# Kernel tuning notes

Hardware: AMD Instinct MI355X
Metric: run time of the kernel (lower is better)

The kernel has to match this reference:

```python
import jax, jax.numpy as jnp
import numpy as np

WEIGHT = 1.0
BOND_CUTOFF = 2.4


def setup_inputs() -> dict:
    key = jax.random.key(0)
    k0, k1, k2, k3, k4, k5 = jax.random.split(key, 6)
    N_TOK, L, B = 512, 3072, 2
    is_ligand = jax.random.randint(k0, (N_TOK,), 0, 2) > 0
    token_bonds = jax.random.randint(k1, (N_TOK, N_TOK), 0, 2) > 0
    atom_to_token_map = jax.random.randint(k2, (L,), 0, N_TOK, dtype=jnp.int32)
    crd_mask_L = jax.random.randint(k3, (B, L), 0, 2) > 0
    X_L = jax.random.normal(k4, (B, L, 3), dtype=jnp.float32)
    X_gt_L = jax.random.normal(k5, (B, L, 3), dtype=jnp.float32)
    return {
        'is_ligand': is_ligand,
        'token_bonds': token_bonds,
        'atom_to_token_map': atom_to_token_map,
        'crd_mask_L': crd_mask_L,
        'X_L': X_L,
        'X_gt_L': X_gt_L,
    }


def _pairwise_sqdist(X):
    # X: [B, L, 3] -> [B, L, L] squared pairwise distances
    d = X[:, :, None, :] - X[:, None, :, :]
    return jnp.sum(d * d, axis=-1)


def reference(is_ligand, token_bonds, atom_to_token_map, crd_mask_L, X_L, X_gt_L):
    # inter-polymer-ligand token pair mask: ligand i, non-ligand j
    inter = is_ligand[:, None] & (~is_ligand)[None, :]          # [T, T]
    pl_bonds = token_bonds & inter                              # [T, T]
    # The original O(n_bonds * L^2) loop is exactly this gather:
    pl_atoms = pl_bonds[atom_to_token_map[:, None], atom_to_token_map[None, :]]  # [L, L]
    crd_mask_LL = crd_mask_L[:, :, None] & crd_mask_L[:, None, :]                # [B, L, L]
    mask = pl_atoms[None, :, :] & crd_mask_LL                                    # [B, L, L]

    # safe sqrt (masked entries set to 1 before sqrt; excluded from loss anyway)
    pred = jnp.sqrt(jnp.where(mask, _pairwise_sqdist(X_L), 1.0))
    gt = jnp.sqrt(jnp.where(mask, _pairwise_sqdist(X_gt_L), 1.0))

    bonded = mask & (gt < BOND_CUTOFF)
    err2 = jnp.where(bonded, jnp.square(pred - gt), 0.0)
    cnt = jnp.maximum(jnp.sum(bonded), 1)
    loss = jnp.sum(err2) / cnt.astype(err2.dtype)
    return (WEIGHT * loss, loss)
```

## Files before the change

### kernel.cpp

```cpp
#include <hip/hip_runtime.h>

#define L 3072
#define NT 512
#define CUT2 5.76f
#define GRID 256
#define BLOCK 1024
#define MAXRPB 12

typedef unsigned int u32;
typedef unsigned long long u64;

__global__ __launch_bounds__(BLOCK) void plbl_main(
    const int* __restrict__ is_ligand,
    const int* __restrict__ token_bonds,
    const int* __restrict__ tokmap,
    const int* __restrict__ crd,
    const float* __restrict__ X,
    const float* __restrict__ Xgt,
    double* __restrict__ part_sum,
    u32* __restrict__ part_cnt)
{
    const int t = threadIdx.x;
    const int lane = t & 63;
    const int wv = t >> 6;

    __shared__ u64 s_lig[8];
    __shared__ u32 s_wtot[2][16];
    __shared__ u32 s_cnts[2];
    __shared__ u32 s_colmeta[3072];
    __shared__ u32 s_rowlist[3072];
    __shared__ u64 s_bond[MAXRPB][8];
    __shared__ __align__(16) float s_rowc[MAXRPB][12];
    __shared__ u32 s_rbits[MAXRPB];
    __shared__ double s_rsum[16];
    __shared__ u32 s_rcnt[16];

    if (t < NT) {
        const bool v = is_ligand[t] != 0;
        const u64 bal = __ballot(v);
        if (lane == 0) s_lig[wv] = bal;
    }
    __syncthreads();

    u32 cc = 0, rc = 0;
    u32 meta[3];
    bool cok[3], rok[3];
    #pragma unroll
    for (int k = 0; k < 3; k++) {
        const int a = t * 3 + k;
        const u32 tok = (u32)tokmap[a];
        const bool lig = (s_lig[tok >> 6] >> (tok & 63)) & 1ULL;
        const u32 m0 = crd[a] != 0;
        const u32 m1 = crd[L + a] != 0;
        const bool any = (m0 | m1) != 0u;
        meta[k] = (u32)a | (tok << 12) | (m0 << 21) | (m1 << 22);
        cok[k] = (!lig) && any;
        rok[k] = lig && any;
        cc += cok[k] ? 1u : 0u;
        rc += rok[k] ? 1u : 0u;
    }

    u32 ci = cc, ri = rc;
    #pragma unroll
    for (int o = 1; o < 64; o <<= 1) {
        u32 cv = __shfl_up(ci, o, 64);
        u32 rv = __shfl_up(ri, o, 64);
        if (lane >= o) { ci += cv; ri += rv; }
    }
    if (lane == 63) { s_wtot[0][wv] = ci; s_wtot[1][wv] = ri; }
    __syncthreads();

    if (wv == 0 && lane < 16) {
        const u32 c = s_wtot[0][lane];
        const u32 r = s_wtot[1][lane];
        u32 cs = c, rs = r;
        #pragma unroll
        for (int o = 1; o < 16; o <<= 1) {
            u32 cv = __shfl_up(cs, o, 64);
            u32 rv = __shfl_up(rs, o, 64);
            if (lane >= o) { cs += cv; rs += rv; }
        }
        s_wtot[0][lane] = cs - c;
        s_wtot[1][lane] = rs - r;
        if (lane == 15) { s_cnts[0] = cs; s_cnts[1] = rs; }
    }
    __syncthreads();

    u32 coff = s_wtot[0][wv] + (ci - cc);
    u32 roff = s_wtot[1][wv] + (ri - rc);
    #pragma unroll
    for (int k = 0; k < 3; k++) {
        if (cok[k]) s_colmeta[coff++] = meta[k];
        if (rok[k]) s_rowlist[roff++] = meta[k];
    }
    __syncthreads();

    const int ncol = (int)s_cnts[0];
    const int nrow = (int)s_cnts[1];

    const int rpb = (nrow + GRID - 1) / GRID;
    const int r0 = blockIdx.x * rpb;
    const int r1 = (r0 + rpb < nrow) ? (r0 + rpb) : nrow;
    const int nr = (r1 > r0) ? (r1 - r0) : 0;

    for (int r = 0; r < nr; r++) {
        const u32 rm = s_rowlist[r0 + r];
        const u32 ta1 = (rm >> 12) & 0x1FF;
        if (t < NT) {
            const bool bv = token_bonds[ta1 * NT + t] != 0;
            const u64 bal = __ballot(bv);
            if (lane == 0) s_bond[r][wv] = bal;
        }
    }
    if (t < nr * 12) {
        const int r = t / 12, c = t % 12;
        const u32 rm = s_rowlist[r0 + r];
        const int a1 = (int)(rm & 0xFFF);
        const int batch = (c % 6) / 3;
        const int axis  = c % 3;
        const float* src = (c < 6) ? X : Xgt;
        s_rowc[r][c] = src[(batch * L + a1) * 3 + axis];
    }
    if (t < nr) s_rbits[t] = (s_rowlist[r0 + t] >> 21) & 3u;
    __syncthreads();

    double acc = 0.0;
    u32 cnt = 0;

    for (int j = t; j < ncol; j += BLOCK) {
        const u32 cm = s_colmeta[j];
        const int a2 = (int)(cm & 0xFFF);
        const u32 tok = (cm >> 12) & 0x1FF;
        const u32 cbits = (cm >> 21) & 3u;
        const u32 bhi = tok >> 6;
        const u64 bsel = 1ULL << (tok & 63);

        const int b0 = 3 * a2;
        const int b1 = 3 * L + 3 * a2;
        const float vx0 = X[b0 + 0], vy0 = X[b0 + 1], vz0 = X[b0 + 2];
        const float vx1 = X[b1 + 0], vy1 = X[b1 + 1], vz1 = X[b1 + 2];
        const float wx0 = Xgt[b0 + 0], wy0 = Xgt[b0 + 1], wz0 = Xgt[b0 + 2];
        const float wx1 = Xgt[b1 + 0], wy1 = Xgt[b1 + 1], wz1 = Xgt[b1 + 2];

        for (int r = 0; r < nr; r++) {
            const bool bond = (s_bond[r][bhi] & bsel) != 0ULL;
            const u32 mb = s_rbits[r] & cbits;

            const float p0x = s_rowc[r][0], p0y = s_rowc[r][1], p0z = s_rowc[r][2];
            const float p1x = s_rowc[r][3], p1y = s_rowc[r][4], p1z = s_rowc[r][5];
            const float g0x = s_rowc[r][6], g0y = s_rowc[r][7], g0z = s_rowc[r][8];
            const float g1x = s_rowc[r][9], g1y = s_rowc[r][10], g1z = s_rowc[r][11];

            const float dgx0 = g0x - wx0, dgy0 = g0y - wy0, dgz0 = g0z - wz0;
            const float gt2_0 = dgx0 * dgx0 + dgy0 * dgy0 + dgz0 * dgz0;
            const float dpx0 = p0x - vx0, dpy0 = p0y - vy0, dpz0 = p0z - vz0;
            const float pr2_0 = dpx0 * dpx0 + dpy0 * dpy0 + dpz0 * dpz0;
            const float d0 = sqrtf(pr2_0) - sqrtf(gt2_0);
            const bool k0 = bond && (mb & 1u) && (gt2_0 < CUT2);
            const float dgx1 = g1x - wx1, dgy1 = g1y - wy1, dgz1 = g1z - wz1;
            const float gt2_1 = dgx1 * dgx1 + dgy1 * dgy1 + dgz1 * dgz1;
            const float dpx1 = p1x - vx1, dpy1 = p1y - vy1, dpz1 = p1z - vz1;
            const float pr2_1 = dpx1 * dpx1 + dpy1 * dpy1 + dpz1 * dpz1;
            const float d1 = sqrtf(pr2_1) - sqrtf(gt2_1);
            const bool k1 = bond && (mb & 2u) && (gt2_1 < CUT2);

            const float e = (k0 ? d0 * d0 : 0.0f) + (k1 ? d1 * d1 : 0.0f);
            acc += (double)e;
            cnt += (k0 ? 1u : 0u) + (k1 ? 1u : 0u);
        }
    }

    #pragma unroll
    for (int o = 32; o > 0; o >>= 1) {
        acc += __shfl_down(acc, o, 64);
        cnt += __shfl_down(cnt, o, 64);
    }
    if (lane == 0) { s_rsum[wv] = acc; s_rcnt[wv] = cnt; }
    __syncthreads();
    if (t == 0) {
        double a = 0.0;
        u32 c = 0;
        #pragma unroll
        for (int i = 0; i < 16; i++) { a += s_rsum[i]; c += s_rcnt[i]; }
        part_sum[blockIdx.x] = a;
        part_cnt[blockIdx.x] = c;
    }
}

__global__ __launch_bounds__(256) void plbl_fin(
    const double* __restrict__ part_sum,
    const u32* __restrict__ part_cnt,
    float* __restrict__ out)
{
    const int t = threadIdx.x;
    const int lane = t & 63;
    const int wv = t >> 6;
    double a = part_sum[t];
    u32 c = part_cnt[t];
    #pragma unroll
    for (int o = 32; o > 0; o >>= 1) {
        a += __shfl_down(a, o, 64);
        c += __shfl_down(c, o, 64);
    }
    __shared__ double s_sum[4];
    __shared__ u32 s_cnt[4];
    if (lane == 0) { s_sum[wv] = a; s_cnt[wv] = c; }
    __syncthreads();
    if (t == 0) {
        const double sum = s_sum[0] + s_sum[1] + s_sum[2] + s_sum[3];
        const u32 cc = s_cnt[0] + s_cnt[1] + s_cnt[2] + s_cnt[3];
        const u32 n = cc ? cc : 1u;
        const float loss = (float)(sum / (double)n);
        out[0] = loss;
        out[1] = loss;
    }
}

extern "C" void kernel_launch(void* const* d_in, const int* in_sizes, int n_in,
                              void* d_out, int out_size, void* d_ws, size_t ws_size,
                              hipStream_t stream) {
    const int*   is_ligand   = (const int*)d_in[0];
    const int*   token_bonds = (const int*)d_in[1];
    const int*   tokmap      = (const int*)d_in[2];
    const int*   crd_mask    = (const int*)d_in[3];
    const float* X           = (const float*)d_in[4];
    const float* Xgt         = (const float*)d_in[5];
    float* out = (float*)d_out;

    char* w = (char*)d_ws;
    double* part_sum = (double*)(w + 0);
    u32*    part_cnt = (u32*)(w + 8 * GRID);

    plbl_main<<<GRID, BLOCK, 0, stream>>>(is_ligand, token_bonds, tokmap,
                                          crd_mask, X, Xgt,
                                          part_sum, part_cnt);
    plbl_fin<<<1, 256, 0, stream>>>(part_sum, part_cnt, out);
}
```

Before: 16.66 us.

## Fuse final reduction into main kernel via cooperative grid sync

Merges the separate finalize kernel into the main kernel, using a cooperative launch and grid-wide sync so that block 0 reduces the per-block partials and writes the loss. It also replaces one block barrier in the prefix scan with per-wave shuffles, and splits the token-bond ballot loading across both halves of the block. The aim is to remove a second kernel launch and some block synchronisation. In exchange it adds cooperative-launch overhead and a grid barrier across 256 blocks of 1024 threads.

After: 52.67 us. +216.1%, slower.

```diff
diff --git a/kernel.cpp b/kernel.cpp
--- a/kernel.cpp
+++ b/kernel.cpp
@@ -1,4 +1,7 @@
 #include <hip/hip_runtime.h>
+#include <hip/hip_cooperative_groups.h>
+
+namespace cg = cooperative_groups;
 
 #define L 3072
 #define NT 512
@@ -10,7 +13,7 @@
 typedef unsigned int u32;
 typedef unsigned long long u64;
 
-__global__ __launch_bounds__(BLOCK) void plbl_main(
+__global__ __launch_bounds__(BLOCK) void plbl_fused(
     const int* __restrict__ is_ligand,
     const int* __restrict__ token_bonds,
     const int* __restrict__ tokmap,
@@ -18,7 +21,8 @@
     const float* __restrict__ X,
     const float* __restrict__ Xgt,
     double* __restrict__ part_sum,
-    u32* __restrict__ part_cnt)
+    u32* __restrict__ part_cnt,
+    float* __restrict__ out)
 {
     const int t = threadIdx.x;
     const int lane = t & 63;
@@ -26,7 +30,6 @@
 
     __shared__ u64 s_lig[8];
     __shared__ u32 s_wtot[2][16];
-    __shared__ u32 s_cnts[2];
     __shared__ u32 s_colmeta[3072];
     __shared__ u32 s_rowlist[3072];
     __shared__ u64 s_bond[MAXRPB][8];
@@ -70,48 +73,50 @@
     if (lane == 63) { s_wtot[0][wv] = ci; s_wtot[1][wv] = ri; }
     __syncthreads();
 
-    if (wv == 0 && lane < 16) {
-        const u32 c = s_wtot[0][lane];
-        const u32 r = s_wtot[1][lane];
-        u32 cs = c, rs = r;
+    u32 cex, rex;
+    int ncol, nrow;
+    {
+        u32 cs = (lane < 16) ? s_wtot[0][lane] : 0u;
+        u32 rs = (lane < 16) ? s_wtot[1][lane] : 0u;
         #pragma unroll
         for (int o = 1; o < 16; o <<= 1) {
             u32 cv = __shfl_up(cs, o, 64);
             u32 rv = __shfl_up(rs, o, 64);
-            if (lane >= o) { cs += cv; rs += rv; }
-        }
-        s_wtot[0][lane] = cs - c;
-        s_wtot[1][lane] = rs - r;
-        if (lane == 15) { s_cnts[0] = cs; s_cnts[1] = rs; }
-    }
-    __syncthreads();
-
-    u32 coff = s_wtot[0][wv] + (ci - cc);
-    u32 roff = s_wtot[1][wv] + (ri - rc);
+            if (lane >= o && lane < 16) { cs += cv; rs += rv; }
+        }
+        cex = (wv == 0) ? 0u : __shfl(cs, wv - 1, 64);
+        rex = (wv == 0) ? 0u : __shfl(rs, wv - 1, 64);
+        ncol = (int)__shfl(cs, 15, 64);
+        nrow = (int)__shfl(rs, 15, 64);
+    }
+
+    u32 coff = cex + (ci - cc);
+    u32 roff = rex + (ri - rc);
     #pragma unroll
     for (int k = 0; k < 3; k++) {
         if (cok[k]) s_colmeta[coff++] = meta[k];
         if (rok[k]) s_rowlist[roff++] = meta[k];
     }
     __syncthreads();
-
-    const int ncol = (int)s_cnts[0];
-    const int nrow = (int)s_cnts[1];
 
     const int rpb = (nrow + GRID - 1) / GRID;
     const int r0 = blockIdx.x * rpb;
     const int r1 = (r0 + rpb < nrow) ? (r0 + rpb) : nrow;
     const int nr = (r1 > r0) ? (r1 - r0) : 0;
 
-    for (int r = 0; r < nr; r++) {
-        const u32 rm = s_rowlist[r0 + r];
-        const u32 ta1 = (rm >> 12) & 0x1FF;
-        if (t < NT) {
-            const bool bv = token_bonds[ta1 * NT + t] != 0;
+    {
+        const int half = wv >> 3;
+        const int w8 = wv & 7;
+        for (int r = half; r < nr; r += 2) {
+            const u32 rm = s_rowlist[r0 + r];
+            const u32 ta1 = (rm >> 12) & 0x1FF;
+            const int tokidx = (w8 << 6) | lane;
+            const bool bv = token_bonds[ta1 * NT + tokidx] != 0;
             const u64 bal = __ballot(bv);
-            if (lane == 0) s_bond[r][wv] = bal;
-        }
-    }
+            if (lane == 0) s_bond[r][w8] = bal;
+        }
+    }
+    if (t >= 512 + 64) {  }
     if (t < nr * 12) {
         const int r = t / 12, c = t % 12;
         const u32 rm = s_rowlist[r0 + r];
@@ -182,37 +187,42 @@
         u32 c = 0;
         #pragma unroll
         for (int i = 0; i < 16; i++) { a += s_rsum[i]; c += s_rcnt[i]; }
-        part_sum[blockIdx.x] = a;
-        part_cnt[blockIdx.x] = c;
-    }
-}
-
-__global__ __launch_bounds__(256) void plbl_fin(
-    const double* __restrict__ part_sum,
-    const u32* __restrict__ part_cnt,
-    float* __restrict__ out)
-{
-    const int t = threadIdx.x;
-    const int lane = t & 63;
-    const int wv = t >> 6;
-    double a = part_sum[t];
-    u32 c = part_cnt[t];
-    #pragma unroll
-    for (int o = 32; o > 0; o >>= 1) {
-        a += __shfl_down(a, o, 64);
-        c += __shfl_down(c, o, 64);
-    }
-    __shared__ double s_sum[4];
-    __shared__ u32 s_cnt[4];
-    if (lane == 0) { s_sum[wv] = a; s_cnt[wv] = c; }
-    __syncthreads();
-    if (t == 0) {
-        const double sum = s_sum[0] + s_sum[1] + s_sum[2] + s_sum[3];
-        const u32 cc = s_cnt[0] + s_cnt[1] + s_cnt[2] + s_cnt[3];
-        const u32 n = cc ? cc : 1u;
-        const float loss = (float)(sum / (double)n);
-        out[0] = loss;
-        out[1] = loss;
+        __hip_atomic_store(&part_sum[blockIdx.x], a, __ATOMIC_RELAXED,
+                           __HIP_MEMORY_SCOPE_AGENT);
+        __hip_atomic_store(&part_cnt[blockIdx.x], c, __ATOMIC_RELAXED,
+                           __HIP_MEMORY_SCOPE_AGENT);
+        asm volatile("s_waitcnt vmcnt(0)" ::: "memory");
+    }
+
+    cg::this_grid().sync();
+
+    if (blockIdx.x == 0) {
+        double a = 0.0;
+        u32 c = 0;
+        if (t < GRID) {
+            a = __hip_atomic_load(&part_sum[t], __ATOMIC_RELAXED,
+                                  __HIP_MEMORY_SCOPE_AGENT);
+            c = __hip_atomic_load(&part_cnt[t], __ATOMIC_RELAXED,
+                                  __HIP_MEMORY_SCOPE_AGENT);
+        }
+        #pragma unroll
+        for (int o = 32; o > 0; o >>= 1) {
+            a += __shfl_down(a, o, 64);
+            c += __shfl_down(c, o, 64);
+        }
+        __syncthreads();
+        if (lane == 0) { s_rsum[wv] = a; s_rcnt[wv] = c; }
+        __syncthreads();
+        if (t == 0) {
+            double sum = 0.0;
+            u32 cc2 = 0;
+            #pragma unroll
+            for (int i = 0; i < 16; i++) { sum += s_rsum[i]; cc2 += s_rcnt[i]; }
+            const u32 n = cc2 ? cc2 : 1u;
+            const float loss = (float)(sum / (double)n);
+            out[0] = loss;
+            out[1] = loss;
+        }
     }
 }
 
@@ -231,8 +241,11 @@
     double* part_sum = (double*)(w + 0);
     u32*    part_cnt = (u32*)(w + 8 * GRID);
 
-    plbl_main<<<GRID, BLOCK, 0, stream>>>(is_ligand, token_bonds, tokmap,
-                                          crd_mask, X, Xgt,
-                                          part_sum, part_cnt);
-    plbl_fin<<<1, 256, 0, stream>>>(part_sum, part_cnt, out);
+    void* args[] = {
+        (void*)&is_ligand, (void*)&token_bonds, (void*)&tokmap,
+        (void*)&crd_mask, (void*)&X, (void*)&Xgt,
+        (void*)&part_sum, (void*)&part_cnt, (void*)&out
+    };
+    hipLaunchCooperativeKernel((const void*)plbl_fused,
+                               dim3(GRID), dim3(BLOCK), args, 0, stream);
 }
```
